# Kernel optimization log

Hardware: AMD Instinct MI355X
Metric: run time of the kernel (lower is better)

## Reference

```python
import jax, jax.numpy as jnp
import numpy as np

LEARNING_RATE = 0.01


def setup_inputs() -> dict:
    key = jax.random.key(0)
    k1, k2 = jax.random.split(key)
    O, D = 512, 128  # output_dim, input_dim; batch must equal output_dim for the broadcast
    x = jax.random.normal(k1, (O, D), dtype=jnp.float32)
    weights = jax.random.normal(k2, (O, O, D), dtype=jnp.float32)
    return {"x": x, "weights": weights}


def reference(x, weights):
    # x: (B, D) with B == O; weights: (O, O, D)
    O = weights.shape[0]
    sigma = O / 2.0
    x = x.reshape(-1, weights.shape[-1])
    diff = weights - x[:, None, :]                      # (O, O, D)
    distances = jnp.sum(diff * diff, axis=-1)            # (O, O)
    winner = jnp.argmin(distances, axis=1)               # (O,)
    neighborhood = jnp.exp(-distances / (2.0 * sigma ** 2))  # (O, O)
    delta = LEARNING_RATE * neighborhood[..., None] * (x[:, None, :] - weights)  # (O, O, D)
    # torch: self.weights.data += torch.sum(delta, dim=0)  -> (O, D) broadcast over rows
    new_weights = weights + jnp.sum(delta, axis=0)        # (O, O, D)
    return winner, new_weights
```

## Files before the change

### kernel.cpp

```cpp
#include <hip/hip_runtime.h>
#include <stdint.h>

#define O_DIM 512
#define D_DIM 128
#define LR 0.01f
#define INV2SIG2 7.62939453125e-6f

#define LDS_GRPS 8
#define HOLD_GRPS 14
#define RR_GRPS 10

typedef float f32x4 __attribute__((ext_vector_type(4)));

__global__ __launch_bounds__(512) void som_fused(
    const float* __restrict__ X,
    const float* __restrict__ W,
    float* __restrict__ dist,
    float* __restrict__ outW)
{
    const int j    = blockIdx.x;
    const int t    = threadIdx.x;
    const int wave = t >> 6;
    const int lane = t & 63;
    const int g    = lane >> 5;
    const int i32  = lane & 31;
    const int d0   = i32 * 4;
    const int rb   = wave * 2 + g;

    __shared__ float ldsW[LDS_GRPS * 16 * D_DIM];
    __shared__ float sacc[8][D_DIM];
    __shared__ float sS[D_DIM];

    f32x4 acc = {0.f, 0.f, 0.f, 0.f};

    #pragma unroll
    for (int bt = 0; bt < 2; ++bt) {
        f32x4 wv[4], xv[4];
        #pragma unroll
        for (int u = 0; u < 4; ++u) {
            const int b = (bt * 4 + u) * 16 + rb;
            wv[u] = *(const f32x4*)(W + ((size_t)b * O_DIM + j) * D_DIM + d0);
            xv[u] = *(const f32x4*)(X + (size_t)b * D_DIM + d0);
        }
        #pragma unroll
        for (int u = 0; u < 4; ++u) {
            const int b = (bt * 4 + u) * 16 + rb;
            const f32x4 dx = wv[u] - xv[u];
            float sum = dx.x * dx.x;
            sum = fmaf(dx.y, dx.y, sum);
            sum = fmaf(dx.z, dx.z, sum);
            sum = fmaf(dx.w, dx.w, sum);
            sum += __shfl_xor(sum, 1, 64);
            sum += __shfl_xor(sum, 2, 64);
            sum += __shfl_xor(sum, 4, 64);
            sum += __shfl_xor(sum, 8, 64);
            sum += __shfl_xor(sum, 16, 64);

            if (i32 == 0) dist[(size_t)b * O_DIM + j] = sum;

            const float c = LR * __expf(-sum * INV2SIG2);
            acc -= c * dx;

            *(f32x4*)(&ldsW[b * D_DIM + d0]) = wv[u];
        }
    }

    f32x4 whold[HOLD_GRPS];
    #pragma unroll
    for (int bt = 0; bt < 4; ++bt) {
        const int n = (bt < 3) ? 4 : 2;
        f32x4 xv[4];
        #pragma unroll
        for (int u = 0; u < 4; ++u) {
            if (u < n) {
                const int idx = bt * 4 + u;
                const int b = (LDS_GRPS + idx) * 16 + rb;
                whold[idx] = *(const f32x4*)(W + ((size_t)b * O_DIM + j) * D_DIM + d0);
                xv[u] = *(const f32x4*)(X + (size_t)b * D_DIM + d0);
            }
        }
        #pragma unroll
        for (int u = 0; u < 4; ++u) {
            if (u < n) {
                const int idx = bt * 4 + u;
                const int b = (LDS_GRPS + idx) * 16 + rb;
                const f32x4 dx = whold[idx] - xv[u];
                float sum = dx.x * dx.x;
                sum = fmaf(dx.y, dx.y, sum);
                sum = fmaf(dx.z, dx.z, sum);
                sum = fmaf(dx.w, dx.w, sum);
                sum += __shfl_xor(sum, 1, 64);
                sum += __shfl_xor(sum, 2, 64);
                sum += __shfl_xor(sum, 4, 64);
                sum += __shfl_xor(sum, 8, 64);
                sum += __shfl_xor(sum, 16, 64);

                if (i32 == 0) dist[(size_t)b * O_DIM + j] = sum;

                const float c = LR * __expf(-sum * INV2SIG2);
                acc -= c * dx;
            }
        }
    }

    #pragma unroll
    for (int bt = 0; bt < 2; ++bt) {
        f32x4 wv[5], xv[5];
        #pragma unroll
        for (int u = 0; u < 5; ++u) {
            const int b = (LDS_GRPS + HOLD_GRPS + bt * 5 + u) * 16 + rb;
            wv[u] = *(const f32x4*)(W + ((size_t)b * O_DIM + j) * D_DIM + d0);
            xv[u] = *(const f32x4*)(X + (size_t)b * D_DIM + d0);
        }
        #pragma unroll
        for (int u = 0; u < 5; ++u) {
            const int b = (LDS_GRPS + HOLD_GRPS + bt * 5 + u) * 16 + rb;
            const f32x4 dx = wv[u] - xv[u];
            float sum = dx.x * dx.x;
            sum = fmaf(dx.y, dx.y, sum);
            sum = fmaf(dx.z, dx.z, sum);
            sum = fmaf(dx.w, dx.w, sum);
            sum += __shfl_xor(sum, 1, 64);
            sum += __shfl_xor(sum, 2, 64);
            sum += __shfl_xor(sum, 4, 64);
            sum += __shfl_xor(sum, 8, 64);
            sum += __shfl_xor(sum, 16, 64);

            if (i32 == 0) dist[(size_t)b * O_DIM + j] = sum;

            const float c = LR * __expf(-sum * INV2SIG2);
            acc -= c * dx;
        }
    }

    acc.x += __shfl_xor(acc.x, 32, 64);
    acc.y += __shfl_xor(acc.y, 32, 64);
    acc.z += __shfl_xor(acc.z, 32, 64);
    acc.w += __shfl_xor(acc.w, 32, 64);

    if (lane < 32) *(f32x4*)(&sacc[wave][d0]) = acc;
    __syncthreads();
    if (t < D_DIM) {
        float v = sacc[0][t];
        #pragma unroll
        for (int w = 1; w < 8; ++w) v += sacc[w][t];
        sS[t] = v;
    }
    __syncthreads();
    const f32x4 s4 = *(const f32x4*)(sS + d0);

    #pragma unroll
    for (int idx = 0; idx < HOLD_GRPS; ++idx) {
        const int b = (LDS_GRPS + idx) * 16 + rb;
        __builtin_nontemporal_store(
            whold[idx] + s4, (f32x4*)(outW + ((size_t)b * O_DIM + j) * D_DIM + d0));
    }
    #pragma unroll 4
    for (int grp = 0; grp < LDS_GRPS; ++grp) {
        const int b = grp * 16 + rb;
        const f32x4 wv = *(const f32x4*)(&ldsW[b * D_DIM + d0]);
        __builtin_nontemporal_store(
            wv + s4, (f32x4*)(outW + ((size_t)b * O_DIM + j) * D_DIM + d0));
    }
    #pragma unroll
    for (int bt = 0; bt < 2; ++bt) {
        f32x4 wx[5];
        #pragma unroll
        for (int u = 0; u < 5; ++u) {
            const int b = (LDS_GRPS + HOLD_GRPS + bt * 5 + u) * 16 + rb;
            wx[u] = *(const f32x4*)(W + ((size_t)b * O_DIM + j) * D_DIM + d0);
        }
        #pragma unroll
        for (int u = 0; u < 5; ++u) {
            const int b = (LDS_GRPS + HOLD_GRPS + bt * 5 + u) * 16 + rb;
            __builtin_nontemporal_store(
                wx[u] + s4, (f32x4*)(outW + ((size_t)b * O_DIM + j) * D_DIM + d0));
        }
    }
}

__global__ __launch_bounds__(64) void som_argmin(
    const float* __restrict__ dist,
    float* __restrict__ out)
{
    const int b = blockIdx.x;
    const int lane = threadIdx.x;
    unsigned long long best = ~0ull;
    #pragma unroll
    for (int k = 0; k < 8; ++k) {
        const int jj = k * 64 + lane;
        const float s = dist[(size_t)b * O_DIM + jj];
        const unsigned long long key =
            ((unsigned long long)__float_as_uint(s) << 32) | (unsigned int)jj;
        best = key < best ? key : best;
    }
    #pragma unroll
    for (int m = 32; m >= 1; m >>= 1) {
        const unsigned long long o = __shfl_xor(best, m, 64);
        best = o < best ? o : best;
    }
    if (lane == 0) out[b] = (float)(unsigned int)(best & 0xFFFFFFFFull);
}


__global__ __launch_bounds__(256) void som_pass1_atomic(
    const float* __restrict__ X, const float* __restrict__ W,
    float* __restrict__ S, unsigned long long* __restrict__ wkey)
{
    const int j = blockIdx.x >> 2, chunk = blockIdx.x & 3;
    const int wave = threadIdx.x >> 6, lane = threadIdx.x & 63;
    const int d0 = lane * 2;
    float accx = 0.f, accy = 0.f;
    const int b_end = chunk * 128 + 128;
    for (int b = chunk * 128 + wave; b < b_end; b += 4) {
        const float2 w2 = *(const float2*)(W + ((size_t)b * O_DIM + j) * D_DIM + d0);
        const float2 x2 = *(const float2*)(X + (size_t)b * D_DIM + d0);
        const float dx = w2.x - x2.x, dy = w2.y - x2.y;
        float s = dx * dx + dy * dy;
        #pragma unroll
        for (int m = 32; m >= 1; m >>= 1) s += __shfl_xor(s, m, 64);
        if (lane == 0)
            atomicMin(&wkey[b], ((unsigned long long)__float_as_uint(s) << 32) | (unsigned)j);
        const float c = LR * __expf(-s * INV2SIG2);
        accx -= c * dx; accy -= c * dy;
    }
    __shared__ float sacc[D_DIM];
    if (threadIdx.x < D_DIM) sacc[threadIdx.x] = 0.f;
    __syncthreads();
    atomicAdd(&sacc[d0], accx); atomicAdd(&sacc[d0 + 1], accy);
    __syncthreads();
    if (threadIdx.x < D_DIM) atomicAdd(&S[(size_t)j * D_DIM + threadIdx.x], sacc[threadIdx.x]);
}

__global__ __launch_bounds__(256) void som_pass2_atomic(
    const float* __restrict__ W, const float* __restrict__ S,
    const unsigned long long* __restrict__ wkey, float* __restrict__ out)
{
    const size_t tid = (size_t)blockIdx.x * blockDim.x + threadIdx.x;
    if (tid < O_DIM) out[tid] = (float)(unsigned int)(wkey[tid] & 0xFFFFFFFFull);
    float* __restrict__ outW = out + O_DIM;
    const size_t total4 = (size_t)O_DIM * O_DIM * D_DIM / 4;
    const size_t stride = (size_t)gridDim.x * blockDim.x;
    for (size_t i = tid; i < total4; i += stride) {
        const size_t e = i * 4;
        const float4 w4 = *(const float4*)(W + e);
        const float4 s4 = *(const float4*)(S + (e & (size_t)(O_DIM * D_DIM - 1)));
        float4 o4 = {w4.x + s4.x, w4.y + s4.y, w4.z + s4.z, w4.w + s4.w};
        *(float4*)(outW + e) = o4;
    }
}

extern "C" void kernel_launch(void* const* d_in, const int* in_sizes, int n_in,
                              void* d_out, int out_size, void* d_ws, size_t ws_size,
                              hipStream_t stream)
{
    const float* X = (const float*)d_in[0];
    const float* W = (const float*)d_in[1];
    float* out = (float*)d_out;

    const size_t DIST_BYTES = (size_t)O_DIM * O_DIM * sizeof(float);

    if (ws_size >= DIST_BYTES) {
        float* dist = (float*)d_ws;
        som_fused <<<dim3(512), dim3(512), 0, stream>>>(X, W, dist, out + O_DIM);
        som_argmin<<<dim3(512), dim3(64),  0, stream>>>(dist, out);
    } else {
        float* S = (float*)d_ws;
        unsigned long long* wkey =
            (unsigned long long*)((char*)d_ws + (size_t)O_DIM * D_DIM * sizeof(float));
        hipMemsetAsync(S, 0, (size_t)O_DIM * D_DIM * sizeof(float), stream);
        hipMemsetAsync(wkey, 0xFF, (size_t)O_DIM * sizeof(unsigned long long), stream);
        som_pass1_atomic<<<dim3(2048), dim3(256), 0, stream>>>(X, W, S, wkey);
        som_pass2_atomic<<<dim3(2048), dim3(256), 0, stream>>>(W, S, wkey, out);
    }
}
```

Before: 55.44 us.

## Process two output columns per block, overlapping column B loads with column A stores

Result: slower. 61.27 us (+10.5%).

```diff
diff --git a/kernel.cpp b/kernel.cpp
--- a/kernel.cpp
+++ b/kernel.cpp
@@ -6,9 +6,8 @@
 #define LR 0.01f
 #define INV2SIG2 7.62939453125e-6f
 
-#define LDS_GRPS 8
+#define LDS_GRPS 18
 #define HOLD_GRPS 14
-#define RR_GRPS 10
 
 typedef float f32x4 __attribute__((ext_vector_type(4)));
 
@@ -18,7 +17,8 @@
     float* __restrict__ dist,
     float* __restrict__ outW)
 {
-    const int j    = blockIdx.x;
+    const int jA   = blockIdx.x * 2;
+    const int jB   = jA + 1;
     const int t    = threadIdx.x;
     const int wave = t >> 6;
     const int lane = t & 63;
@@ -34,17 +34,17 @@
     f32x4 acc = {0.f, 0.f, 0.f, 0.f};
 
     #pragma unroll
-    for (int bt = 0; bt < 2; ++bt) {
-        f32x4 wv[4], xv[4];
-        #pragma unroll
-        for (int u = 0; u < 4; ++u) {
-            const int b = (bt * 4 + u) * 16 + rb;
-            wv[u] = *(const f32x4*)(W + ((size_t)b * O_DIM + j) * D_DIM + d0);
+    for (int bt = 0; bt < 3; ++bt) {
+        f32x4 wv[6], xv[6];
+        #pragma unroll
+        for (int u = 0; u < 6; ++u) {
+            const int b = (bt * 6 + u) * 16 + rb;
+            wv[u] = *(const f32x4*)(W + ((size_t)b * O_DIM + jA) * D_DIM + d0);
             xv[u] = *(const f32x4*)(X + (size_t)b * D_DIM + d0);
         }
         #pragma unroll
-        for (int u = 0; u < 4; ++u) {
-            const int b = (bt * 4 + u) * 16 + rb;
+        for (int u = 0; u < 6; ++u) {
+            const int b = (bt * 6 + u) * 16 + rb;
             const f32x4 dx = wv[u] - xv[u];
             float sum = dx.x * dx.x;
             sum = fmaf(dx.y, dx.y, sum);
@@ -55,16 +55,12 @@
             sum += __shfl_xor(sum, 4, 64);
             sum += __shfl_xor(sum, 8, 64);
             sum += __shfl_xor(sum, 16, 64);
-
-            if (i32 == 0) dist[(size_t)b * O_DIM + j] = sum;
-
+            if (i32 == 0) dist[(size_t)b * O_DIM + jA] = sum;
             const float c = LR * __expf(-sum * INV2SIG2);
             acc -= c * dx;
-
             *(f32x4*)(&ldsW[b * D_DIM + d0]) = wv[u];
         }
     }
-
     f32x4 whold[HOLD_GRPS];
     #pragma unroll
     for (int bt = 0; bt < 4; ++bt) {
@@ -75,7 +71,7 @@
             if (u < n) {
                 const int idx = bt * 4 + u;
                 const int b = (LDS_GRPS + idx) * 16 + rb;
-                whold[idx] = *(const f32x4*)(W + ((size_t)b * O_DIM + j) * D_DIM + d0);
+                whold[idx] = *(const f32x4*)(W + ((size_t)b * O_DIM + jA) * D_DIM + d0);
                 xv[u] = *(const f32x4*)(X + (size_t)b * D_DIM + d0);
             }
         }
@@ -94,42 +90,10 @@
                 sum += __shfl_xor(sum, 4, 64);
                 sum += __shfl_xor(sum, 8, 64);
                 sum += __shfl_xor(sum, 16, 64);
-
-                if (i32 == 0) dist[(size_t)b * O_DIM + j] = sum;
-
+                if (i32 == 0) dist[(size_t)b * O_DIM + jA] = sum;
                 const float c = LR * __expf(-sum * INV2SIG2);
                 acc -= c * dx;
             }
-        }
-    }
-
-    #pragma unroll
-    for (int bt = 0; bt < 2; ++bt) {
-        f32x4 wv[5], xv[5];
-        #pragma unroll
-        for (int u = 0; u < 5; ++u) {
-            const int b = (LDS_GRPS + HOLD_GRPS + bt * 5 + u) * 16 + rb;
-            wv[u] = *(const f32x4*)(W + ((size_t)b * O_DIM + j) * D_DIM + d0);
-            xv[u] = *(const f32x4*)(X + (size_t)b * D_DIM + d0);
-        }
-        #pragma unroll
-        for (int u = 0; u < 5; ++u) {
-            const int b = (LDS_GRPS + HOLD_GRPS + bt * 5 + u) * 16 + rb;
-            const f32x4 dx = wv[u] - xv[u];
-            float sum = dx.x * dx.x;
-            sum = fmaf(dx.y, dx.y, sum);
-            sum = fmaf(dx.z, dx.z, sum);
-            sum = fmaf(dx.w, dx.w, sum);
-            sum += __shfl_xor(sum, 1, 64);
-            sum += __shfl_xor(sum, 2, 64);
-            sum += __shfl_xor(sum, 4, 64);
-            sum += __shfl_xor(sum, 8, 64);
-            sum += __shfl_xor(sum, 16, 64);
-
-            if (i32 == 0) dist[(size_t)b * O_DIM + j] = sum;
-
-            const float c = LR * __expf(-sum * INV2SIG2);
-            acc -= c * dx;
         }
     }
 
@@ -137,7 +101,6 @@
     acc.y += __shfl_xor(acc.y, 32, 64);
     acc.z += __shfl_xor(acc.z, 32, 64);
     acc.w += __shfl_xor(acc.w, 32, 64);
-
     if (lane < 32) *(f32x4*)(&sacc[wave][d0]) = acc;
     __syncthreads();
     if (t < D_DIM) {
@@ -147,35 +110,111 @@
         sS[t] = v;
     }
     __syncthreads();
-    const f32x4 s4 = *(const f32x4*)(sS + d0);
+    const f32x4 sA4 = *(const f32x4*)(sS + d0);
+
+    acc = (f32x4){0.f, 0.f, 0.f, 0.f};
+
+    #pragma unroll
+    for (int bt = 0; bt < 4; ++bt) {
+        const int n = (bt < 3) ? 4 : 2;
+        f32x4 xv[4];
+        #pragma unroll
+        for (int u = 0; u < 4; ++u) {
+            if (u < n) {
+                const int idx = bt * 4 + u;
+                const int b = (LDS_GRPS + idx) * 16 + rb;
+                __builtin_nontemporal_store(
+                    whold[idx] + sA4,
+                    (f32x4*)(outW + ((size_t)b * O_DIM + jA) * D_DIM + d0));
+                whold[idx] = *(const f32x4*)(W + ((size_t)b * O_DIM + jB) * D_DIM + d0);
+                xv[u] = *(const f32x4*)(X + (size_t)b * D_DIM + d0);
+            }
+        }
+        #pragma unroll
+        for (int u = 0; u < 4; ++u) {
+            if (u < n) {
+                const int idx = bt * 4 + u;
+                const int b = (LDS_GRPS + idx) * 16 + rb;
+                const f32x4 dx = whold[idx] - xv[u];
+                float sum = dx.x * dx.x;
+                sum = fmaf(dx.y, dx.y, sum);
+                sum = fmaf(dx.z, dx.z, sum);
+                sum = fmaf(dx.w, dx.w, sum);
+                sum += __shfl_xor(sum, 1, 64);
+                sum += __shfl_xor(sum, 2, 64);
+                sum += __shfl_xor(sum, 4, 64);
+                sum += __shfl_xor(sum, 8, 64);
+                sum += __shfl_xor(sum, 16, 64);
+                if (i32 == 0) dist[(size_t)b * O_DIM + jB] = sum;
+                const float c = LR * __expf(-sum * INV2SIG2);
+                acc -= c * dx;
+            }
+        }
+    }
+    #pragma unroll
+    for (int bt = 0; bt < 5; ++bt) {
+        const int n = (bt < 4) ? 4 : 2;
+        f32x4 wv[4], xv[4];
+        #pragma unroll
+        for (int u = 0; u < 4; ++u) {
+            if (u < n) {
+                const int b = (bt * 4 + u) * 16 + rb;
+                const f32x4 wa = *(const f32x4*)(&ldsW[b * D_DIM + d0]);
+                __builtin_nontemporal_store(
+                    wa + sA4, (f32x4*)(outW + ((size_t)b * O_DIM + jA) * D_DIM + d0));
+                wv[u] = *(const f32x4*)(W + ((size_t)b * O_DIM + jB) * D_DIM + d0);
+                xv[u] = *(const f32x4*)(X + (size_t)b * D_DIM + d0);
+            }
+        }
+        #pragma unroll
+        for (int u = 0; u < 4; ++u) {
+            if (u < n) {
+                const int b = (bt * 4 + u) * 16 + rb;
+                *(f32x4*)(&ldsW[b * D_DIM + d0]) = wv[u];
+                const f32x4 dx = wv[u] - xv[u];
+                float sum = dx.x * dx.x;
+                sum = fmaf(dx.y, dx.y, sum);
+                sum = fmaf(dx.z, dx.z, sum);
+                sum = fmaf(dx.w, dx.w, sum);
+                sum += __shfl_xor(sum, 1, 64);
+                sum += __shfl_xor(sum, 2, 64);
+                sum += __shfl_xor(sum, 4, 64);
+                sum += __shfl_xor(sum, 8, 64);
+                sum += __shfl_xor(sum, 16, 64);
+                if (i32 == 0) dist[(size_t)b * O_DIM + jB] = sum;
+                const float c = LR * __expf(-sum * INV2SIG2);
+                acc -= c * dx;
+            }
+        }
+    }
+
+    acc.x += __shfl_xor(acc.x, 32, 64);
+    acc.y += __shfl_xor(acc.y, 32, 64);
+    acc.z += __shfl_xor(acc.z, 32, 64);
+    acc.w += __shfl_xor(acc.w, 32, 64);
+    if (lane < 32) *(f32x4*)(&sacc[wave][d0]) = acc;
+    __syncthreads();
+    if (t < D_DIM) {
+        float v = sacc[0][t];
+        #pragma unroll
+        for (int w = 1; w < 8; ++w) v += sacc[w][t];
+        sS[t] = v;
+    }
+    __syncthreads();
+    const f32x4 sB4 = *(const f32x4*)(sS + d0);
 
     #pragma unroll
     for (int idx = 0; idx < HOLD_GRPS; ++idx) {
         const int b = (LDS_GRPS + idx) * 16 + rb;
         __builtin_nontemporal_store(
-            whold[idx] + s4, (f32x4*)(outW + ((size_t)b * O_DIM + j) * D_DIM + d0));
-    }
-    #pragma unroll 4
+            whold[idx] + sB4, (f32x4*)(outW + ((size_t)b * O_DIM + jB) * D_DIM + d0));
+    }
+    #pragma unroll 6
     for (int grp = 0; grp < LDS_GRPS; ++grp) {
         const int b = grp * 16 + rb;
         const f32x4 wv = *(const f32x4*)(&ldsW[b * D_DIM + d0]);
         __builtin_nontemporal_store(
-            wv + s4, (f32x4*)(outW + ((size_t)b * O_DIM + j) * D_DIM + d0));
-    }
-    #pragma unroll
-    for (int bt = 0; bt < 2; ++bt) {
-        f32x4 wx[5];
-        #pragma unroll
-        for (int u = 0; u < 5; ++u) {
-            const int b = (LDS_GRPS + HOLD_GRPS + bt * 5 + u) * 16 + rb;
-            wx[u] = *(const f32x4*)(W + ((size_t)b * O_DIM + j) * D_DIM + d0);
-        }
-        #pragma unroll
-        for (int u = 0; u < 5; ++u) {
-            const int b = (LDS_GRPS + HOLD_GRPS + bt * 5 + u) * 16 + rb;
-            __builtin_nontemporal_store(
-                wx[u] + s4, (f32x4*)(outW + ((size_t)b * O_DIM + j) * D_DIM + d0));
-        }
+            wv + sB4, (f32x4*)(outW + ((size_t)b * O_DIM + jB) * D_DIM + d0));
     }
 }
 
@@ -262,7 +301,7 @@
 
     if (ws_size >= DIST_BYTES) {
         float* dist = (float*)d_ws;
-        som_fused <<<dim3(512), dim3(512), 0, stream>>>(X, W, dist, out + O_DIM);
+        som_fused <<<dim3(256), dim3(512), 0, stream>>>(X, W, dist, out + O_DIM);
         som_argmin<<<dim3(512), dim3(64),  0, stream>>>(dist, out);
     } else {
         float* S = (float*)d_ws;
```
